# Optimization experiments

Hardware: AMD Instinct MI355X
Metric: run time of the kernel (lower is better)

## Reference

```python
import jax, jax.numpy as jnp
import numpy as np

NUM_HEADS = 4
GROUPS = 8
EPS = 1e-5


def setup_inputs() -> dict:
    key = jax.random.key(0)
    ks = jax.random.split(key, 8)
    B, C, H, W = 8, 512, 64, 64
    L, E = 77, 768
    std = 0.02
    return {
        "x": jax.random.normal(ks[0], (B, C, H, W), jnp.float32),
        "text_emb": jax.random.normal(ks[1], (B, L, E), jnp.float32),
        "attention_mask": jax.random.randint(ks[2], (B, L), 0, 2, jnp.int32),
        "Wq_w": jax.random.normal(ks[3], (C, C), jnp.float32) * std,
        "Wq_b": jnp.zeros((C,), jnp.float32),
        "Wk_w": jax.random.normal(ks[4], (C, E), jnp.float32) * std,
        "Wk_b": jnp.zeros((C,), jnp.float32),
        "Wv_w": jax.random.normal(ks[5], (C, E), jnp.float32) * std,
        "Wv_b": jnp.zeros((C,), jnp.float32),
        "gn_scale": jnp.ones((C,), jnp.float32),
        "gn_bias": jnp.zeros((C,), jnp.float32),
    }


def reference(x, text_emb, attention_mask, Wq_w, Wq_b, Wk_w, Wk_b, Wv_w, Wv_b, gn_scale, gn_bias):
    B, C, H, W = x.shape
    dh = C // NUM_HEADS
    scale = dh ** -0.5

    # [B, HW, C] queries from image features
    x_flat = x.reshape(B, C, H * W).transpose(0, 2, 1)
    Q = x_flat @ Wq_w.T + Wq_b                 # [B, S, C]
    K = text_emb @ Wk_w.T + Wk_b               # [B, L, C]
    V = text_emb @ Wv_w.T + Wv_b               # [B, L, C]

    def split_heads(t):
        Bt, T, _ = t.shape
        return t.reshape(Bt, T, NUM_HEADS, dh).transpose(0, 2, 1, 3)  # [B, h, T, dh]

    Qh, Kh, Vh = split_heads(Q), split_heads(K), split_heads(V)

    scores = jnp.einsum("bhqd,bhkd->bhqk", Qh, Kh) * scale  # [B, h, S, L]
    mask = (attention_mask == 0)[:, None, None, :]
    scores = jnp.where(mask, -jnp.inf, scores)
    probs = jax.nn.softmax(scores, axis=-1)
    # dropout layers are identity in eval mode
    attn = jnp.einsum("bhqk,bhkd->bhqd", probs, Vh)          # [B, h, S, dh]

    out = attn.transpose(0, 2, 1, 3).reshape(B, H * W, C)    # [B, S, C]
    out = out.transpose(0, 2, 1).reshape(B, C, H, W)

    # GroupNorm(8 groups, affine) over (C/G, H, W) per group
    g = out.reshape(B, GROUPS, -1)
    mean = g.mean(axis=-1, keepdims=True)
    var = g.var(axis=-1, keepdims=True)
    g = (g - mean) * jax.lax.rsqrt(var + EPS)
    out = g.reshape(B, C, H, W) * gn_scale[None, :, None, None] + gn_bias[None, :, None, None]
    return out
```

## Files before the change

kernel.cpp:

```cpp
#include <hip/hip_runtime.h>
#include <hip/hip_bf16.h>
#include <cstdint>


typedef __attribute__((ext_vector_type(8))) short short8;
typedef __attribute__((ext_vector_type(4))) short short4v;
typedef __attribute__((ext_vector_type(4))) float f32x4;

#define DEV __device__ __forceinline__

DEV float bf2f(unsigned short u){ union{uint32_t i; float f;} x; x.i = ((uint32_t)u) << 16; return x.f; }
DEV unsigned short f2bf(float f){ __hip_bfloat16 h = __float2bfloat16(f); return *reinterpret_cast<unsigned short*>(&h); }
DEV short8 ld8(const unsigned short* p){ return *reinterpret_cast<const short8*>(p); }
DEV f32x4 ldf4(const float* p){ return *reinterpret_cast<const f32x4*>(p); }

#if defined(__has_builtin)
#if __has_builtin(__builtin_amdgcn_global_load_lds)
#define HAVE_ASYNC_LDS 1
#endif
#endif

__global__ __launch_bounds__(256) void k_fat(const float* __restrict__ x,
                                             unsigned short* __restrict__ xT,
                                             const float* __restrict__ text,
                                             const float* __restrict__ Wk,
                                             const float* __restrict__ Wkb,
                                             const float* __restrict__ Wv,
                                             const float* __restrict__ Wvb,
                                             unsigned short* __restrict__ wsK,
                                             unsigned short* __restrict__ wsVt,
                                             const float* __restrict__ Wq,
                                             unsigned short* __restrict__ wsWq,
                                             int b0, int s_base, int slen, int SB){
  __shared__ unsigned short U[10368];
  const int tid = threadIdx.x;
  const int bx = blockIdx.x, by = blockIdx.y, bz = blockIdx.z;
  const int bg = b0 + bz;

  if (bx < 64){
    if (bx * 64 >= slen) return;
    unsigned short* t = U;
    const int s0 = s_base + bx * 64, c0 = by * 64;
    #pragma unroll
    for (int it = 0; it < 2; ++it){
      int slot = tid + it * 256;
      int r = slot >> 3, sg = slot & 7;
      int sw = sg ^ (r >> 3);
      const float* src = &x[((size_t)(bg * 512 + c0 + r)) * 4096 + s0 + sg * 8];
      f32x4 a = ldf4(src), b = ldf4(src + 4);
      short8 v;
      #pragma unroll
      for (int j = 0; j < 4; ++j){ v[j] = (short)f2bf(a[j]); v[j + 4] = (short)f2bf(b[j]); }
      *reinterpret_cast<short8*>(&t[r * 72 + sw * 8]) = v;
    }
    __syncthreads();
    #pragma unroll
    for (int it = 0; it < 2; ++it){
      int slot = tid + it * 256;
      int j = slot >> 3, i8 = slot & 7;
      short8 v;
      #pragma unroll
      for (int q = 0; q < 8; ++q){
        int c = i8 * 8 + q;
        int sw = (j >> 3) ^ i8;
        v[q] = (short)t[c * 72 + sw * 8 + (j & 7)];
      }
      *reinterpret_cast<short8*>(&xT[((size_t)(bz * slen) + bx * 64 + j) * 512 + c0 + i8 * 8]) = v;
    }
  } else if (bx < 66){
    unsigned short* At = U;
    unsigned short* Bt = U + 5760;
    const int wave = tid >> 6, lane = tid & 63;
    const int m16 = lane & 15, quad = lane >> 4;
    const int uc = (bx - 64) * 8 + by;
    const int u0 = uc * 64;
    const bool isK = (u0 < 512);
    const float* W  = isK ? Wk  : Wv;
    const float* Wb = isK ? Wkb : Wvb;
    const int c0 = u0 & 511;
    const int c  = c0 + wave * 16 + m16;
    f32x4 acc[5];
    #pragma unroll
    for (int mt = 0; mt < 5; ++mt) acc[mt] = (f32x4){0.f, 0.f, 0.f, 0.f};
    for (int kc = 0; kc < 12; ++kc){
      const int e0 = kc * 64;
      #pragma unroll
      for (int it = 0; it < 9; ++it){
        int slot = tid + it * 256;
        if (slot < 1280){
          int row = slot >> 4, e4 = (slot & 15) * 4;
          f32x4 v = (row < 77) ? ldf4(&text[((size_t)(bg * 77 + row)) * 768 + e0 + e4])
                               : (f32x4){0.f, 0.f, 0.f, 0.f};
          short4v o;
          #pragma unroll
          for (int j = 0; j < 4; ++j) o[j] = (short)f2bf(v[j]);
          *reinterpret_cast<short4v*>(&At[row * 72 + e4]) = o;
        } else {
          int bs = slot - 1280;
          int row = bs >> 4, e4 = (bs & 15) * 4;
          f32x4 v = ldf4(&W[((size_t)(c0 + row)) * 768 + e0 + e4]);
          short4v o;
          #pragma unroll
          for (int j = 0; j < 4; ++j) o[j] = (short)f2bf(v[j]);
          *reinterpret_cast<short4v*>(&Bt[row * 72 + e4]) = o;
        }
      }
      __syncthreads();
      #pragma unroll
      for (int kk = 0; kk < 64; kk += 32){
        short8 bf_ = *reinterpret_cast<const short8*>(&Bt[(wave * 16 + m16) * 72 + kk + quad * 8]);
        #pragma unroll
        for (int mt = 0; mt < 5; ++mt){
          short8 af_ = *reinterpret_cast<const short8*>(&At[(mt * 16 + m16) * 72 + kk + quad * 8]);
          acc[mt] = __builtin_amdgcn_mfma_f32_16x16x32_bf16(af_, bf_, acc[mt], 0, 0, 0);
        }
      }
      __syncthreads();
    }
    const float bias = Wb[c];
    if (isK){
      #pragma unroll
      for (int mt = 0; mt < 5; ++mt)
        #pragma unroll
        for (int r = 0; r < 4; ++r){
          int l = mt * 16 + quad * 4 + r;
          if (l < 77) wsK[((size_t)(bz * 77 + l)) * 512 + c] = f2bf(acc[mt][r] + bias);
        }
    } else {
      unsigned short* vr = &wsVt[((size_t)(bz * 512 + c)) * 96];
      #pragma unroll
      for (int mt = 0; mt < 5; ++mt){
        short4v pk;
        #pragma unroll
        for (int r = 0; r < 4; ++r) pk[r] = (short)f2bf(acc[mt][r] + bias);
        *reinterpret_cast<short4v*>(&vr[mt * 16 + quad * 4]) = pk;
      }
      short4v z = {};
      *reinterpret_cast<short4v*>(&vr[80 + quad * 4]) = z;
    }
  } else {
    const int nb = 8 * SB;
    const int p  = by + bz * 8;
    const int chunk = 262144 / nb;
    for (int i = p * chunk + tid * 4; i < (p + 1) * chunk; i += 1024){
      f32x4 v = ldf4(&Wq[i]);
      short4v o;
      #pragma unroll
      for (int j = 0; j < 4; ++j) o[j] = (short)f2bf(v[j]);
      *reinterpret_cast<short4v*>(&wsWq[i]) = o;
    }
  }
}

__global__ __launch_bounds__(256, 4) void k2_attn(const unsigned short* __restrict__ xT,
                                                  const unsigned short* __restrict__ wsK,
                                                  const unsigned short* __restrict__ wsVt,
                                                  const int* __restrict__ amask,
                                                  const unsigned short* __restrict__ wsWq,
                                                  const float* __restrict__ Wqb,
                                                  float* __restrict__ out,
                                                  float* __restrict__ gnacc,
                                                  int b0, int s_base, int slen){
  __shared__ unsigned short arena[17408];
  __shared__ float maskf[96];
  unsigned short* ldsA = arena;
  unsigned short* ldsB = arena + 8192;
  unsigned short* Qt   = arena;
  unsigned short* Pt   = arena;

  const int tid = threadIdx.x;
  const int wave = tid >> 6, lane = tid & 63;
  const int m16 = lane & 15, quad = lane >> 4;
  const int st = blockIdx.x, h = blockIdx.y, bz = blockIdx.z;
  const int bg = b0 + bz;
  const int s_glob = s_base + st * 128;
  const int R0 = (wave >> 1) * 64, C0 = (wave & 1) * 64;

  if (tid < 96){
    int l = tid;
    float mbv = -30000.f;
    if (l < 77 && amask[bg * 77 + l] != 0) mbv = 0.f;
    maskf[l] = mbv;
  }

  f32x4 acc[4][4];
  #pragma unroll
  for (int mt = 0; mt < 4; ++mt)
    #pragma unroll
    for (int nt = 0; nt < 4; ++nt) acc[mt][nt] = (f32x4){0.f, 0.f, 0.f, 0.f};
  const unsigned short* Aglob = wsWq + (size_t)(h * 128) * 512;
  const unsigned short* Bglob = xT + ((size_t)bz * slen + st * 128) * 512;
  for (int kc = 0; kc < 8; ++kc){
    #pragma unroll
    for (int it = 0; it < 4; ++it){
      int slot = tid + it * 256;
      int row = slot >> 3;
      int sc8 = (slot & 7) ^ (row & 7);
      const unsigned short* ga = &Aglob[(size_t)row * 512 + kc * 64 + sc8 * 8];
#ifdef HAVE_ASYNC_LDS
      __builtin_amdgcn_global_load_lds((const __attribute__((address_space(1))) void*)ga,
                                       (__attribute__((address_space(3))) void*)&ldsA[(it * 256 + wave * 64) * 8],
                                       16, 0, 0);
#else
      *reinterpret_cast<short8*>(&ldsA[slot * 8]) = ld8(ga);
#endif
    }
    #pragma unroll
    for (int it = 0; it < 4; ++it){
      int slot = tid + it * 256;
      int row = slot >> 3;
      int sc8 = (slot & 7) ^ (row & 7);
      const unsigned short* gb = &Bglob[(size_t)row * 512 + kc * 64 + sc8 * 8];
#ifdef HAVE_ASYNC_LDS
      __builtin_amdgcn_global_load_lds((const __attribute__((address_space(1))) void*)gb,
                                       (__attribute__((address_space(3))) void*)&ldsB[(it * 256 + wave * 64) * 8],
                                       16, 0, 0);
#else
      *reinterpret_cast<short8*>(&ldsB[slot * 8]) = ld8(gb);
#endif
    }
    __syncthreads();
    #pragma unroll
    for (int kk = 0; kk < 64; kk += 32){
      short8 af[4], bfr[4];
      #pragma unroll
      for (int mt = 0; mt < 4; ++mt){
        int r = R0 + mt * 16 + m16;
        af[mt] = *reinterpret_cast<const short8*>(&ldsA[r * 64 + (((kk >> 3) + quad) ^ (r & 7)) * 8]);
      }
      #pragma unroll
      for (int nt = 0; nt < 4; ++nt){
        int r = C0 + nt * 16 + m16;
        bfr[nt] = *reinterpret_cast<const short8*>(&ldsB[r * 64 + (((kk >> 3) + quad) ^ (r & 7)) * 8]);
      }
      #pragma unroll
      for (int mt = 0; mt < 4; ++mt)
        #pragma unroll
        for (int nt = 0; nt < 4; ++nt)
          acc[mt][nt] = __builtin_amdgcn_mfma_f32_16x16x32_bf16(af[mt], bfr[nt], acc[mt][nt], 0, 0, 0);
    }
    __syncthreads();
  }
  {
    float qb[4][4];
    #pragma unroll
    for (int mt = 0; mt < 4; ++mt)
      #pragma unroll
      for (int r = 0; r < 4; ++r) qb[mt][r] = Wqb[h * 128 + R0 + mt * 16 + quad * 4 + r];
    #pragma unroll
    for (int mt = 0; mt < 4; ++mt)
      #pragma unroll
      for (int nt = 0; nt < 4; ++nt){
        int sl = C0 + nt * 16 + m16;
        short4v pk;
        #pragma unroll
        for (int r = 0; r < 4; ++r) pk[r] = (short)f2bf(acc[mt][nt][r] + qb[mt][r]);
        *reinterpret_cast<short4v*>(&Qt[sl * 136 + R0 + mt * 16 + quad * 4]) = pk;
      }
  }
  __syncthreads();

  f32x4 acc2[5][2];
  #pragma unroll
  for (int mt = 0; mt < 5; ++mt){ acc2[mt][0] = (f32x4){0.f,0.f,0.f,0.f}; acc2[mt][1] = (f32x4){0.f,0.f,0.f,0.f}; }
  const int cb = wave * 32;
  const unsigned short* Kb = wsK + (size_t)(bz * 77) * 512 + h * 128;
  #pragma unroll
  for (int ks = 0; ks < 4; ++ks){
    short8 bq[2];
    #pragma unroll
    for (int nt = 0; nt < 2; ++nt)
      bq[nt] = *reinterpret_cast<const short8*>(&Qt[(cb + nt * 16 + m16) * 136 + ks * 32 + quad * 8]);
    #pragma unroll
    for (int mt = 0; mt < 5; ++mt){
      int l = mt * 16 + m16;
      short8 ak = {};
      if (l < 77) ak = ld8(&Kb[(size_t)l * 512 + ks * 32 + quad * 8]);
      #pragma unroll
      for (int nt = 0; nt < 2; ++nt)
        acc2[mt][nt] = __builtin_amdgcn_mfma_f32_16x16x32_bf16(ak, bq[nt], acc2[mt][nt], 0, 0, 0);
    }
  }
  __syncthreads();

  {
    const float scale = 0.08838834764831845f;
    float mb[5][4];
    #pragma unroll
    for (int mt = 0; mt < 5; ++mt)
      #pragma unroll
      for (int r = 0; r < 4; ++r) mb[mt][r] = maskf[mt * 16 + quad * 4 + r];
    #pragma unroll
    for (int nt = 0; nt < 2; ++nt){
      float sv[5][4]; float mx = -3e38f;
      #pragma unroll
      for (int mt = 0; mt < 5; ++mt)
        #pragma unroll
        for (int r = 0; r < 4; ++r){
          float v = acc2[mt][nt][r] * scale + mb[mt][r];
          sv[mt][r] = v; mx = fmaxf(mx, v);
        }
      mx = fmaxf(mx, __shfl_xor(mx, 16)); mx = fmaxf(mx, __shfl_xor(mx, 32));
      float sum = 0.f;
      #pragma unroll
      for (int mt = 0; mt < 5; ++mt)
        #pragma unroll
        for (int r = 0; r < 4; ++r){ float e = __expf(sv[mt][r] - mx); sv[mt][r] = e; sum += e; }
      sum += __shfl_xor(sum, 16); sum += __shfl_xor(sum, 32);
      float inv = 1.0f / sum;
      int sl = cb + nt * 16 + m16;
      #pragma unroll
      for (int mt = 0; mt < 5; ++mt){
        short4v pk;
        #pragma unroll
        for (int r = 0; r < 4; ++r) pk[r] = (short)f2bf(sv[mt][r] * inv);
        *reinterpret_cast<short4v*>(&Pt[sl * 104 + mt * 16 + quad * 4]) = pk;
      }
      short4v z = {};
      *reinterpret_cast<short4v*>(&Pt[sl * 104 + 80 + quad * 4]) = z;
    }
  }
  __syncthreads();

  f32x4 acc3[4][4];
  #pragma unroll
  for (int mt = 0; mt < 4; ++mt)
    #pragma unroll
    for (int nt = 0; nt < 4; ++nt) acc3[mt][nt] = (f32x4){0.f, 0.f, 0.f, 0.f};
  const unsigned short* Vb = wsVt + (size_t)(bz * 512 + h * 128) * 96;
  #pragma unroll
  for (int ks = 0; ks < 3; ++ks){
    short8 av[4], bp[4];
    #pragma unroll
    for (int mt = 0; mt < 4; ++mt)
      av[mt] = ld8(&Vb[(size_t)(R0 + mt * 16 + m16) * 96 + ks * 32 + quad * 8]);
    #pragma unroll
    for (int nt = 0; nt < 4; ++nt)
      bp[nt] = *reinterpret_cast<const short8*>(&Pt[(C0 + nt * 16 + m16) * 104 + ks * 32 + quad * 8]);
    #pragma unroll
    for (int mt = 0; mt < 4; ++mt)
      #pragma unroll
      for (int nt = 0; nt < 4; ++nt)
        acc3[mt][nt] = __builtin_amdgcn_mfma_f32_16x16x32_bf16(av[mt], bp[nt], acc3[mt][nt], 0, 0, 0);
  }
  float sum = 0.f, ssq = 0.f;
  #pragma unroll
  for (int mt = 0; mt < 4; ++mt)
    #pragma unroll
    for (int nt = 0; nt < 4; ++nt){
      int sidx = s_glob + C0 + nt * 16 + m16;
      #pragma unroll
      for (int r = 0; r < 4; ++r){
        float v = acc3[mt][nt][r];
        sum += v; ssq += v * v;
        int d = h * 128 + R0 + mt * 16 + quad * 4 + r;
        out[(size_t)(bg * 512 + d) * 4096 + sidx] = v;
      }
    }
  #pragma unroll
  for (int off = 1; off < 64; off <<= 1){ sum += __shfl_xor(sum, off); ssq += __shfl_xor(ssq, off); }
  if (lane == 0){
    int g = h * 2 + (R0 >> 6);
    atomicAdd(&gnacc[(bg * 8 + g) * 2],     sum);
    atomicAdd(&gnacc[(bg * 8 + g) * 2 + 1], ssq);
  }
}

__global__ __launch_bounds__(256) void k3_gn(float* __restrict__ out,
                                             const float* __restrict__ gnacc,
                                             const float* __restrict__ gns,
                                             const float* __restrict__ gnb){
  const int bx = blockIdx.x;
  const int b = bx >> 9, c = bx & 511;
  const int g = c >> 6;
  const float s  = gnacc[(b * 8 + g) * 2];
  const float ss = gnacc[(b * 8 + g) * 2 + 1];
  const float invN = 1.f / 262144.f;
  const float mean = s * invN;
  const float var  = ss * invN - mean * mean;
  const float rstd = rsqrtf(fmaxf(var, 0.f) + 1e-5f);
  const float a  = rstd * gns[c];
  const float bb = gnb[c] - mean * a;
  const size_t base = (size_t)bx * 4096;
  #pragma unroll
  for (int p = 0; p < 4; ++p){
    size_t off = base + p * 1024 + threadIdx.x * 4;
    f32x4 v = ldf4(&out[off]);
    f32x4 o;
    #pragma unroll
    for (int j = 0; j < 4; ++j) o[j] = v[j] * a + bb;
    *reinterpret_cast<f32x4*>(&out[off]) = o;
  }
}

extern "C" void kernel_launch(void* const* d_in, const int* in_sizes, int n_in,
                              void* d_out, int out_size, void* d_ws, size_t ws_size,
                              hipStream_t stream){
  (void)in_sizes; (void)n_in; (void)out_size;
  const float* x    = (const float*)d_in[0];
  const float* text = (const float*)d_in[1];
  const int*   am   = (const int*)d_in[2];
  const float* Wq   = (const float*)d_in[3];
  const float* Wqb  = (const float*)d_in[4];
  const float* Wk   = (const float*)d_in[5];
  const float* Wkb  = (const float*)d_in[6];
  const float* Wv   = (const float*)d_in[7];
  const float* Wvb  = (const float*)d_in[8];
  const float* gns  = (const float*)d_in[9];
  const float* gnb  = (const float*)d_in[10];
  float* out = (float*)d_out;

  auto need = [](int SB, int SLEN) -> size_t {
    return 512ull + 524288ull + (size_t)SB * 78848ull + (size_t)SB * 98304ull
         + (size_t)SB * SLEN * 1024ull;
  };
  int SB = 8, SLEN = 4096;
  if      (ws_size >= need(8, 4096)) { SB = 8; SLEN = 4096; }
  else if (ws_size >= need(4, 4096)) { SB = 4; SLEN = 4096; }
  else if (ws_size >= need(2, 4096)) { SB = 2; SLEN = 4096; }
  else if (ws_size >= need(1, 4096)) { SB = 1; SLEN = 4096; }
  else if (ws_size >= need(1, 1024)) { SB = 1; SLEN = 1024; }
  else                               { SB = 1; SLEN = 256;  }

  uint8_t* ws = (uint8_t*)d_ws;
  float*          gnacc = (float*)ws;
  unsigned short* wsWq  = (unsigned short*)(ws + 512);
  unsigned short* wsK   = wsWq + 512 * 512;
  unsigned short* wsVt  = wsK  + (size_t)SB * 77 * 512;
  unsigned short* xT    = wsVt + (size_t)SB * 512 * 96;

  hipMemsetAsync(gnacc, 0, 128 * sizeof(float), stream);
  for (int b0 = 0; b0 < 8; b0 += SB){
    for (int s_base = 0; s_base < 4096; s_base += SLEN){
      k_fat<<<dim3(67, 8, SB), 256, 0, stream>>>(x, xT, text, Wk, Wkb, Wv, Wvb,
                                                 wsK, wsVt, Wq, wsWq, b0, s_base, SLEN, SB);
      k2_attn<<<dim3(SLEN / 128, 4, SB), 256, 0, stream>>>(xT, wsK, wsVt, am, wsWq, Wqb,
                                                           out, gnacc, b0, s_base, SLEN);
    }
  }
  k3_gn<<<4096, 256, 0, stream>>>(out, gnacc, gns, gnb);
}
```

Baseline: 136.0 us.

## Load Q-projection MFMA operands directly from global memory, bypassing LDS staging

```diff
diff --git a/kernel.cpp b/kernel.cpp
--- a/kernel.cpp
+++ b/kernel.cpp
@@ -13,12 +13,6 @@
 DEV unsigned short f2bf(float f){ __hip_bfloat16 h = __float2bfloat16(f); return *reinterpret_cast<unsigned short*>(&h); }
 DEV short8 ld8(const unsigned short* p){ return *reinterpret_cast<const short8*>(p); }
 DEV f32x4 ldf4(const float* p){ return *reinterpret_cast<const f32x4*>(p); }
-
-#if defined(__has_builtin)
-#if __has_builtin(__builtin_amdgcn_global_load_lds)
-#define HAVE_ASYNC_LDS 1
-#endif
-#endif
 
 __global__ __launch_bounds__(256) void k_fat(const float* __restrict__ x,
                                              unsigned short* __restrict__ xT,
@@ -163,8 +157,6 @@
                                                   int b0, int s_base, int slen){
   __shared__ unsigned short arena[17408];
   __shared__ float maskf[96];
-  unsigned short* ldsA = arena;
-  unsigned short* ldsB = arena + 8192;
   unsigned short* Qt   = arena;
   unsigned short* Pt   = arena;
 
@@ -188,58 +180,26 @@
   for (int mt = 0; mt < 4; ++mt)
     #pragma unroll
     for (int nt = 0; nt < 4; ++nt) acc[mt][nt] = (f32x4){0.f, 0.f, 0.f, 0.f};
-  const unsigned short* Aglob = wsWq + (size_t)(h * 128) * 512;
-  const unsigned short* Bglob = xT + ((size_t)bz * slen + st * 128) * 512;
-  for (int kc = 0; kc < 8; ++kc){
-    #pragma unroll
-    for (int it = 0; it < 4; ++it){
-      int slot = tid + it * 256;
-      int row = slot >> 3;
-      int sc8 = (slot & 7) ^ (row & 7);
-      const unsigned short* ga = &Aglob[(size_t)row * 512 + kc * 64 + sc8 * 8];
-#ifdef HAVE_ASYNC_LDS
-      __builtin_amdgcn_global_load_lds((const __attribute__((address_space(1))) void*)ga,
-                                       (__attribute__((address_space(3))) void*)&ldsA[(it * 256 + wave * 64) * 8],
-                                       16, 0, 0);
-#else
-      *reinterpret_cast<short8*>(&ldsA[slot * 8]) = ld8(ga);
-#endif
-    }
-    #pragma unroll
-    for (int it = 0; it < 4; ++it){
-      int slot = tid + it * 256;
-      int row = slot >> 3;
-      int sc8 = (slot & 7) ^ (row & 7);
-      const unsigned short* gb = &Bglob[(size_t)row * 512 + kc * 64 + sc8 * 8];
-#ifdef HAVE_ASYNC_LDS
-      __builtin_amdgcn_global_load_lds((const __attribute__((address_space(1))) void*)gb,
-                                       (__attribute__((address_space(3))) void*)&ldsB[(it * 256 + wave * 64) * 8],
-                                       16, 0, 0);
-#else
-      *reinterpret_cast<short8*>(&ldsB[slot * 8]) = ld8(gb);
-#endif
-    }
-    __syncthreads();
-    #pragma unroll
-    for (int kk = 0; kk < 64; kk += 32){
-      short8 af[4], bfr[4];
-      #pragma unroll
-      for (int mt = 0; mt < 4; ++mt){
-        int r = R0 + mt * 16 + m16;
-        af[mt] = *reinterpret_cast<const short8*>(&ldsA[r * 64 + (((kk >> 3) + quad) ^ (r & 7)) * 8]);
-      }
-      #pragma unroll
-      for (int nt = 0; nt < 4; ++nt){
-        int r = C0 + nt * 16 + m16;
-        bfr[nt] = *reinterpret_cast<const short8*>(&ldsB[r * 64 + (((kk >> 3) + quad) ^ (r & 7)) * 8]);
-      }
-      #pragma unroll
-      for (int mt = 0; mt < 4; ++mt)
-        #pragma unroll
-        for (int nt = 0; nt < 4; ++nt)
-          acc[mt][nt] = __builtin_amdgcn_mfma_f32_16x16x32_bf16(af[mt], bfr[nt], acc[mt][nt], 0, 0, 0);
-    }
-    __syncthreads();
+  const unsigned short* Ab[4];
+  const unsigned short* Bb[4];
+  #pragma unroll
+  for (int mt = 0; mt < 4; ++mt)
+    Ab[mt] = wsWq + (size_t)(h * 128 + R0 + mt * 16 + m16) * 512 + quad * 8;
+  #pragma unroll
+  for (int nt = 0; nt < 4; ++nt)
+    Bb[nt] = xT + ((size_t)bz * slen + st * 128 + C0 + nt * 16 + m16) * 512 + quad * 8;
+  #pragma unroll 4
+  for (int ks = 0; ks < 16; ++ks){
+    short8 af[4], bfr[4];
+    #pragma unroll
+    for (int mt = 0; mt < 4; ++mt) af[mt] = ld8(Ab[mt] + ks * 32);
+    #pragma unroll
+    for (int nt = 0; nt < 4; ++nt) bfr[nt] = ld8(Bb[nt] + ks * 32);
+    #pragma unroll
+    for (int mt = 0; mt < 4; ++mt)
+      #pragma unroll
+      for (int nt = 0; nt < 4; ++nt)
+        acc[mt][nt] = __builtin_amdgcn_mfma_f32_16x16x32_bf16(af[mt], bfr[nt], acc[mt][nt], 0, 0, 0);
   }
   {
     float qb[4][4];
```

Result: slower. 176.4 us (+29.7%).

## Fold Wq into K per head so scores come directly from x

Applied to the files above, without the earlier changes.

```diff
diff --git a/kernel.cpp b/kernel.cpp
--- a/kernel.cpp
+++ b/kernel.cpp
@@ -30,7 +30,7 @@
                                              unsigned short* __restrict__ wsK,
                                              unsigned short* __restrict__ wsVt,
                                              const float* __restrict__ Wq,
-                                             unsigned short* __restrict__ wsWq,
+                                             unsigned short* __restrict__ wsWqT,
                                              int b0, int s_base, int slen, int SB){
   __shared__ unsigned short U[10368];
   const int tid = threadIdx.x;
@@ -139,34 +139,116 @@
       *reinterpret_cast<short4v*>(&vr[80 + quad * 4]) = z;
     }
   } else {
+    unsigned short* t = U;
     const int nb = 8 * SB;
     const int p  = by + bz * 8;
-    const int chunk = 262144 / nb;
-    for (int i = p * chunk + tid * 4; i < (p + 1) * chunk; i += 1024){
-      f32x4 v = ldf4(&Wq[i]);
-      short4v o;
-      #pragma unroll
-      for (int j = 0; j < 4; ++j) o[j] = (short)f2bf(v[j]);
-      *reinterpret_cast<short4v*>(&wsWq[i]) = o;
+    for (int tile = p; tile < 64; tile += nb){
+      const int ti = tile >> 3, tj = tile & 7;
+      #pragma unroll
+      for (int it = 0; it < 2; ++it){
+        int slot = tid + it * 256;
+        int r = slot >> 3, sg = slot & 7;
+        int sw = sg ^ (r >> 3);
+        const float* src = &Wq[((size_t)(tj * 64 + r)) * 512 + ti * 64 + sg * 8];
+        f32x4 a = ldf4(src), b2 = ldf4(src + 4);
+        short8 v;
+        #pragma unroll
+        for (int j = 0; j < 4; ++j){ v[j] = (short)f2bf(a[j]); v[j + 4] = (short)f2bf(b2[j]); }
+        *reinterpret_cast<short8*>(&t[r * 72 + sw * 8]) = v;
+      }
+      __syncthreads();
+      #pragma unroll
+      for (int it = 0; it < 2; ++it){
+        int slot = tid + it * 256;
+        int j = slot >> 3, i8 = slot & 7;
+        short8 v;
+        #pragma unroll
+        for (int q = 0; q < 8; ++q){
+          int dd = i8 * 8 + q;
+          int sw = (j >> 3) ^ i8;
+          v[q] = (short)t[dd * 72 + sw * 8 + (j & 7)];
+        }
+        *reinterpret_cast<short8*>(&wsWqT[((size_t)(ti * 64 + j)) * 512 + tj * 64 + i8 * 8]) = v;
+      }
+      __syncthreads();
     }
   }
 }
 
-__global__ __launch_bounds__(256, 4) void k2_attn(const unsigned short* __restrict__ xT,
-                                                  const unsigned short* __restrict__ wsK,
+__global__ __launch_bounds__(256) void k1b(const unsigned short* __restrict__ wsWqT,
+                                           const unsigned short* __restrict__ wsK,
+                                           const float* __restrict__ Wqb,
+                                           unsigned short* __restrict__ wsKWq,
+                                           float* __restrict__ kbias){
+  const int tid = threadIdx.x;
+  const int wave = tid >> 6, lane = tid & 63;
+  const int m16 = lane & 15, quad = lane >> 4;
+  const int cq = blockIdx.x, h = blockIdx.y, bz = blockIdx.z;
+  const int cbase = cq * 128 + wave * 32;
+
+  f32x4 acc[2][5];
+  #pragma unroll
+  for (int mt = 0; mt < 2; ++mt)
+    #pragma unroll
+    for (int nt = 0; nt < 5; ++nt) acc[mt][nt] = (f32x4){0.f, 0.f, 0.f, 0.f};
+
+  #pragma unroll
+  for (int ks = 0; ks < 4; ++ks){
+    short8 aw[2];
+    #pragma unroll
+    for (int mt = 0; mt < 2; ++mt)
+      aw[mt] = ld8(&wsWqT[(size_t)(cbase + mt * 16 + m16) * 512 + h * 128 + ks * 32 + quad * 8]);
+    #pragma unroll
+    for (int nt = 0; nt < 5; ++nt){
+      int l = nt * 16 + m16;
+      short8 bk = {};
+      if (l < 77) bk = ld8(&wsK[((size_t)(bz * 77 + l)) * 512 + h * 128 + ks * 32 + quad * 8]);
+      #pragma unroll
+      for (int mt = 0; mt < 2; ++mt)
+        acc[mt][nt] = __builtin_amdgcn_mfma_f32_16x16x32_bf16(aw[mt], bk, acc[mt][nt], 0, 0, 0);
+    }
+  }
+  #pragma unroll
+  for (int mt = 0; mt < 2; ++mt)
+    #pragma unroll
+    for (int nt = 0; nt < 5; ++nt){
+      int l = nt * 16 + m16;
+      short4v pk;
+      #pragma unroll
+      for (int r = 0; r < 4; ++r) pk[r] = (short)f2bf(acc[mt][nt][r]);
+      *reinterpret_cast<short4v*>(&wsKWq[((size_t)((bz * 4 + h) * 80 + l)) * 512 + cbase + mt * 16 + quad * 4]) = pk;
+    }
+  if (cq == 0 && tid < 80){
+    int l = tid;
+    float kb = 0.f;
+    if (l < 77){
+      #pragma unroll
+      for (int d = 0; d < 128; d += 8){
+        short8 kv = ld8(&wsK[((size_t)(bz * 77 + l)) * 512 + h * 128 + d]);
+        f32x4 wa = ldf4(&Wqb[h * 128 + d]);
+        f32x4 wb = ldf4(&Wqb[h * 128 + d + 4]);
+        #pragma unroll
+        for (int j = 0; j < 4; ++j){
+          kb += bf2f((unsigned short)kv[j]) * wa[j];
+          kb += bf2f((unsigned short)kv[j + 4]) * wb[j];
+        }
+      }
+    }
+    kbias[(bz * 4 + h) * 80 + l] = kb;
+  }
+}
+
+__global__ __launch_bounds__(256, 3) void k2_attn(const unsigned short* __restrict__ xT,
+                                                  const unsigned short* __restrict__ wsKWq,
                                                   const unsigned short* __restrict__ wsVt,
                                                   const int* __restrict__ amask,
-                                                  const unsigned short* __restrict__ wsWq,
-                                                  const float* __restrict__ Wqb,
+                                                  const float* __restrict__ kbias,
                                                   float* __restrict__ out,
                                                   float* __restrict__ gnacc,
                                                   int b0, int s_base, int slen){
-  __shared__ unsigned short arena[17408];
+  __shared__ unsigned short arena[26624];
   __shared__ float maskf[96];
-  unsigned short* ldsA = arena;
-  unsigned short* ldsB = arena + 8192;
-  unsigned short* Qt   = arena;
-  unsigned short* Pt   = arena;
+  unsigned short* Pt = arena;
 
   const int tid = threadIdx.x;
   const int wave = tid >> 6, lane = tid & 63;
@@ -175,116 +257,86 @@
   const int bg = b0 + bz;
   const int s_glob = s_base + st * 128;
   const int R0 = (wave >> 1) * 64, C0 = (wave & 1) * 64;
+  const int sw0 = wave * 32;
+  const float scale = 0.08838834764831845f;
 
   if (tid < 96){
     int l = tid;
     float mbv = -30000.f;
-    if (l < 77 && amask[bg * 77 + l] != 0) mbv = 0.f;
+    if (l < 77 && amask[bg * 77 + l] != 0) mbv = kbias[(bz * 4 + h) * 80 + l] * scale;
     maskf[l] = mbv;
   }
 
-  f32x4 acc[4][4];
-  #pragma unroll
-  for (int mt = 0; mt < 4; ++mt)
-    #pragma unroll
-    for (int nt = 0; nt < 4; ++nt) acc[mt][nt] = (f32x4){0.f, 0.f, 0.f, 0.f};
-  const unsigned short* Aglob = wsWq + (size_t)(h * 128) * 512;
-  const unsigned short* Bglob = xT + ((size_t)bz * slen + st * 128) * 512;
+  const unsigned short* Abase = wsKWq + (size_t)((bz * 4 + h) * 80) * 512;
+  const unsigned short* Bbase = xT + ((size_t)bz * slen + st * 128) * 512;
+
+  f32x4 acc2[5][2];
+  #pragma unroll
+  for (int mt = 0; mt < 5; ++mt){ acc2[mt][0] = (f32x4){0.f,0.f,0.f,0.f}; acc2[mt][1] = (f32x4){0.f,0.f,0.f,0.f}; }
+
+  auto stage = [&](int kc, int buf){
+    const int sbase = buf * 13312;
+    #pragma unroll
+    for (int it = 0; it < 7; ++it){
+      const int ubase = it * 256 + wave * 64;
+      if (ubase < 1664){
+        const int u = ubase + lane;
+        const unsigned short* src;
+        if (u < 640){
+          int l = u >> 3, pos = (u & 7) ^ (l & 7);
+          src = Abase + (size_t)l * 512 + kc * 64 + pos * 8;
+        } else {
+          int v = u - 640;
+          int s = v >> 3, pos = (v & 7) ^ (s & 7);
+          src = Bbase + (size_t)s * 512 + kc * 64 + pos * 8;
+        }
+#ifdef HAVE_ASYNC_LDS
+        __builtin_amdgcn_global_load_lds((const __attribute__((address_space(1))) void*)src,
+                                         (__attribute__((address_space(3))) void*)&arena[sbase + ubase * 8],
+                                         16, 0, 0);
+#else
+        *reinterpret_cast<short8*>(&arena[sbase + (ubase + lane) * 8]) = ld8(src);
+#endif
+      }
+    }
+  };
+
+  auto compute = [&](int buf){
+    const int ab = buf * 13312;
+    const int bb = ab + 5120;
+    #pragma unroll
+    for (int kk = 0; kk < 2; ++kk){
+      short8 af[5], bfr[2];
+      #pragma unroll
+      for (int mt = 0; mt < 5; ++mt){
+        int l = mt * 16 + m16;
+        int p = (kk * 4 + quad) ^ (l & 7);
+        af[mt] = *reinterpret_cast<const short8*>(&arena[ab + l * 64 + p * 8]);
+      }
+      #pragma unroll
+      for (int nt = 0; nt < 2; ++nt){
+        int s = sw0 + nt * 16 + m16;
+        int p = (kk * 4 + quad) ^ (s & 7);
+        bfr[nt] = *reinterpret_cast<const short8*>(&arena[bb + s * 64 + p * 8]);
+      }
+      #pragma unroll
+      for (int mt = 0; mt < 5; ++mt)
+        #pragma unroll
+        for (int nt = 0; nt < 2; ++nt)
+          acc2[mt][nt] = __builtin_amdgcn_mfma_f32_16x16x32_bf16(af[mt], bfr[nt], acc2[mt][nt], 0, 0, 0);
+    }
+  };
+
+  stage(0, 0);
+  __syncthreads();
+  #pragma unroll
   for (int kc = 0; kc < 8; ++kc){
-    #pragma unroll
-    for (int it = 0; it < 4; ++it){
-      int slot = tid + it * 256;
-      int row = slot >> 3;
-      int sc8 = (slot & 7) ^ (row & 7);
-      const unsigned short* ga = &Aglob[(size_t)row * 512 + kc * 64 + sc8 * 8];
-#ifdef HAVE_ASYNC_LDS
-      __builtin_amdgcn_global_load_lds((const __attribute__((address_space(1))) void*)ga,
-                                       (__attribute__((address_space(3))) void*)&ldsA[(it * 256 + wave * 64) * 8],
-                                       16, 0, 0);
-#else
-      *reinterpret_cast<short8*>(&ldsA[slot * 8]) = ld8(ga);
-#endif
-    }
-    #pragma unroll
-    for (int it = 0; it < 4; ++it){
-      int slot = tid + it * 256;
-      int row = slot >> 3;
-      int sc8 = (slot & 7) ^ (row & 7);
-      const unsigned short* gb = &Bglob[(size_t)row * 512 + kc * 64 + sc8 * 8];
-#ifdef HAVE_ASYNC_LDS
-      __builtin_amdgcn_global_load_lds((const __attribute__((address_space(1))) void*)gb,
-                                       (__attribute__((address_space(3))) void*)&ldsB[(it * 256 + wave * 64) * 8],
-                                       16, 0, 0);
-#else
-      *reinterpret_cast<short8*>(&ldsB[slot * 8]) = ld8(gb);
-#endif
-    }
+    if (kc < 7) stage(kc + 1, (kc + 1) & 1);
+    compute(kc & 1);
     __syncthreads();
-    #pragma unroll
-    for (int kk = 0; kk < 64; kk += 32){
-      short8 af[4], bfr[4];
-      #pragma unroll
-      for (int mt = 0; mt < 4; ++mt){
-        int r = R0 + mt * 16 + m16;
-        af[mt] = *reinterpret_cast<const short8*>(&ldsA[r * 64 + (((kk >> 3) + quad) ^ (r & 7)) * 8]);
-      }
-      #pragma unroll
-      for (int nt = 0; nt < 4; ++nt){
-        int r = C0 + nt * 16 + m16;
-        bfr[nt] = *reinterpret_cast<const short8*>(&ldsB[r * 64 + (((kk >> 3) + quad) ^ (r & 7)) * 8]);
-      }
-      #pragma unroll
-      for (int mt = 0; mt < 4; ++mt)
-        #pragma unroll
-        for (int nt = 0; nt < 4; ++nt)
-          acc[mt][nt] = __builtin_amdgcn_mfma_f32_16x16x32_bf16(af[mt], bfr[nt], acc[mt][nt], 0, 0, 0);
-    }
-    __syncthreads();
-  }
+  }
+
   {
-    float qb[4][4];
-    #pragma unroll
-    for (int mt = 0; mt < 4; ++mt)
-      #pragma unroll
-      for (int r = 0; r < 4; ++r) qb[mt][r] = Wqb[h * 128 + R0 + mt * 16 + quad * 4 + r];
-    #pragma unroll
-    for (int mt = 0; mt < 4; ++mt)
-      #pragma unroll
-      for (int nt = 0; nt < 4; ++nt){
-        int sl = C0 + nt * 16 + m16;
-        short4v pk;
-        #pragma unroll
-        for (int r = 0; r < 4; ++r) pk[r] = (short)f2bf(acc[mt][nt][r] + qb[mt][r]);
-        *reinterpret_cast<short4v*>(&Qt[sl * 136 + R0 + mt * 16 + quad * 4]) = pk;
-      }
-  }
-  __syncthreads();
-
-  f32x4 acc2[5][2];
-  #pragma unroll
-  for (int mt = 0; mt < 5; ++mt){ acc2[mt][0] = (f32x4){0.f,0.f,0.f,0.f}; acc2[mt][1] = (f32x4){0.f,0.f,0.f,0.f}; }
-  const int cb = wave * 32;
-  const unsigned short* Kb = wsK + (size_t)(bz * 77) * 512 + h * 128;
-  #pragma unroll
-  for (int ks = 0; ks < 4; ++ks){
-    short8 bq[2];
-    #pragma unroll
-    for (int nt = 0; nt < 2; ++nt)
-      bq[nt] = *reinterpret_cast<const short8*>(&Qt[(cb + nt * 16 + m16) * 136 + ks * 32 + quad * 8]);
-    #pragma unroll
-    for (int mt = 0; mt < 5; ++mt){
-      int l = mt * 16 + m16;
-      short8 ak = {};
-      if (l < 77) ak = ld8(&Kb[(size_t)l * 512 + ks * 32 + quad * 8]);
-      #pragma unroll
-      for (int nt = 0; nt < 2; ++nt)
-        acc2[mt][nt] = __builtin_amdgcn_mfma_f32_16x16x32_bf16(ak, bq[nt], acc2[mt][nt], 0, 0, 0);
-    }
-  }
-  __syncthreads();
-
-  {
-    const float scale = 0.08838834764831845f;
     float mb[5][4];
     #pragma unroll
     for (int mt = 0; mt < 5; ++mt)
@@ -308,7 +360,7 @@
         for (int r = 0; r < 4; ++r){ float e = __expf(sv[mt][r] - mx); sv[mt][r] = e; sum += e; }
       sum += __shfl_xor(sum, 16); sum += __shfl_xor(sum, 32);
       float inv = 1.0f / sum;
-      int sl = cb + nt * 16 + m16;
+      int sl = sw0 + nt * 16 + m16;
       #pragma unroll
       for (int mt = 0; mt < 5; ++mt){
         short4v pk;
@@ -411,8 +463,7 @@
   float* out = (float*)d_out;
 
   auto need = [](int SB, int SLEN) -> size_t {
-    return 512ull + 524288ull + (size_t)SB * 78848ull + (size_t)SB * 98304ull
-         + (size_t)SB * SLEN * 1024ull;
+    return 512ull + 524288ull + (size_t)SB * 506112ull + (size_t)SB * SLEN * 1024ull;
   };
   int SB = 8, SLEN = 4096;
   if      (ws_size >= need(8, 4096)) { SB = 8; SLEN = 4096; }
@@ -424,17 +475,21 @@
 
   uint8_t* ws = (uint8_t*)d_ws;
   float*          gnacc = (float*)ws;
-  unsigned short* wsWq  = (unsigned short*)(ws + 512);
-  unsigned short* wsK   = wsWq + 512 * 512;
+  unsigned short* wsWqT = (unsigned short*)(ws + 512);
+  unsigned short* wsK   = wsWqT + 512 * 512;
   unsigned short* wsVt  = wsK  + (size_t)SB * 77 * 512;
-  unsigned short* xT    = wsVt + (size_t)SB * 512 * 96;
+  unsigned short* wsKWq = wsVt + (size_t)SB * 512 * 96;
+  float*          kbias = (float*)(wsKWq + (size_t)SB * 4 * 80 * 512);
+  unsigned short* xT    = (unsigned short*)(kbias + (size_t)SB * 4 * 80);
 
   hipMemsetAsync(gnacc, 0, 128 * sizeof(float), stream);
   for (int b0 = 0; b0 < 8; b0 += SB){
     for (int s_base = 0; s_base < 4096; s_base += SLEN){
       k_fat<<<dim3(67, 8, SB), 256, 0, stream>>>(x, xT, text, Wk, Wkb, Wv, Wvb,
-                                                 wsK, wsVt, Wq, wsWq, b0, s_base, SLEN, SB);
-      k2_attn<<<dim3(SLEN / 128, 4, SB), 256, 0, stream>>>(xT, wsK, wsVt, am, wsWq, Wqb,
+                                                 wsK, wsVt, Wq, wsWqT, b0, s_base, SLEN, SB);
+      if (s_base == 0)
+        k1b<<<dim3(4, 4, SB), 256, 0, stream>>>(wsWqT, wsK, Wqb, wsKWq, kbias);
+      k2_attn<<<dim3(SLEN / 128, 4, SB), 256, 0, stream>>>(xT, wsKWq, wsVt, am, kbias,
                                                            out, gnacc, b0, s_base, SLEN);
     }
   }
```

Measured after the change: 137.5 us. Within noise of the previous version (+1.1%).
